# Performance work log

Hardware: AMD Instinct MI355X
Metric: run time of the kernel (lower is better)

## Reference

```python
import jax, jax.numpy as jnp
import numpy as np

# TuckerLinear: in_features = out_features = 4096, num_modes = 3
IN_SHAPE = (16, 16, 16)    # get_shape(4096, 3)
OUT_SHAPE = (16, 16, 16)
IN_FEATURES = 4096
OUT_FEATURES = 4096


def setup_inputs() -> dict:
    key = jax.random.key(0)
    ks = jax.random.split(key, 12)
    B, S = 4, 4096
    x = jax.random.normal(ks[0], (B, S, IN_FEATURES), dtype=jnp.float32)
    core = jax.random.normal(ks[1], (8, 8, 8, 8, 8, 8), dtype=jnp.float32) * 0.05
    fi0 = jax.random.normal(ks[2], (16, 8), dtype=jnp.float32) * 0.3
    fi1 = jax.random.normal(ks[3], (16, 8), dtype=jnp.float32) * 0.3
    fi2 = jax.random.normal(ks[4], (16, 8), dtype=jnp.float32) * 0.3
    fo0 = jax.random.normal(ks[5], (16, 8), dtype=jnp.float32) * 0.3
    fo1 = jax.random.normal(ks[6], (16, 8), dtype=jnp.float32) * 0.3
    fo2 = jax.random.normal(ks[7], (16, 8), dtype=jnp.float32) * 0.3
    bias = jax.random.normal(ks[8], (OUT_FEATURES,), dtype=jnp.float32) * 0.01
    per_dim_scale = jnp.ones((OUT_FEATURES,), dtype=jnp.float32)
    alpha = jnp.ones((1,), dtype=jnp.float32)
    input_perm = jax.random.permutation(ks[9], IN_FEATURES).astype(jnp.int32)
    return dict(x=x, core=core, fi0=fi0, fi1=fi1, fi2=fi2,
                fo0=fo0, fo1=fo1, fo2=fo2,
                per_dim_scale=per_dim_scale, alpha=alpha, bias=bias,
                input_perm=input_perm)


def reference(x, core, fi0, fi1, fi2, fo0, fo1, fo2,
              per_dim_scale, alpha, bias, input_perm):
    batch_dims = x.shape[:-1]
    # 1. input channel permutation (spectral reordering)
    xp = jnp.take(x, input_perm, axis=-1)
    # 2. reshape to expose input modes: (N, 16, 16, 16)
    t = xp.reshape(-1, *IN_SHAPE)
    # 3. contract each input mode with its factor (16 -> 8)
    t = jnp.einsum('nabc,ap->npbc', t, fi0)
    t = jnp.einsum('npbc,bq->npqc', t, fi1)
    t = jnp.einsum('npqc,cr->npqr', t, fi2)
    # 4. contract with core over all input-rank modes: (N,8,8,8) -> (N,8,8,8)
    t = jnp.einsum('npqr,xyzpqr->nxyz', t, core)
    # 5. contract each output mode with its factor (8 -> 16)
    t = jnp.einsum('nxyz,Xx->nXyz', t, fo0)
    t = jnp.einsum('nXyz,Yy->nXYz', t, fo1)
    t = jnp.einsum('nXYz,Zz->nXYZ', t, fo2)
    # 6. flatten output modes, scale, bias
    out = t.reshape(-1, OUT_FEATURES)
    out = out * per_dim_scale * alpha + bias
    return out.reshape(*batch_dims, OUT_FEATURES)
```

## Files before the change

kernel.cpp:

```cpp
#include <hip/hip_runtime.h>
#include <stdint.h>

#define NROWS 16384
#define D 4096

typedef __bf16 bf16x8 __attribute__((ext_vector_type(8)));
typedef float  f32x4  __attribute__((ext_vector_type(4)));

__device__ inline unsigned short f2bf(float f) {
    unsigned u = __float_as_uint(f);
    u += 0x7fffu + ((u >> 16) & 1u);
    return (unsigned short)(u >> 16);
}

__global__ __launch_bounds__(256) void k_corebf(const float* __restrict__ core,
                                                unsigned int* __restrict__ cb) {
    const int o = blockIdx.x;
    const int kp = threadIdx.x;
    float2 v = *(const float2*)&core[o * 512 + 2 * kp];
    cb[((size_t)(kp >> 2) * 512 + o) * 4 + (kp & 3)] =
        (unsigned)f2bf(v.x) | ((unsigned)f2bf(v.y) << 16);
}

__global__ __launch_bounds__(256, 5) void k_t3(const float* __restrict__ x,
                                               const float* __restrict__ fi0,
                                               const float* __restrict__ fi1,
                                               const float* __restrict__ fi2,
                                               const int* __restrict__ perm,
                                               unsigned int* __restrict__ t3out) {
    __shared__ float xr[4096];
    __shared__ float t1[2048];
    __shared__ float t2[1024];
    __shared__ float fac[3][128];

    const int tid = threadIdx.x;
    const int n = blockIdx.x;

    {
        const int h = tid & 127;
        fac[0][h] = fi0[h];
        fac[1][h] = fi1[h];
        fac[2][h] = fi2[h];
    }
    int pj[16];
    #pragma unroll
    for (int j = 0; j < 16; ++j) pj[j] = perm[j * 256 + tid];

    {
        const float4* src = (const float4*)(x + (size_t)n * D);
        #pragma unroll
        for (int i = 0; i < 4; ++i) {
            const int c = i * 256 + tid;
            __builtin_amdgcn_global_load_lds(
                (const __attribute__((address_space(1))) void*)(src + c),
                (__attribute__((address_space(3))) void*)(&xr[c * 4]),
                16, 0, 0);
        }
    }
    asm volatile("s_waitcnt vmcnt(0) lgkmcnt(0)" ::: "memory");
    __builtin_amdgcn_s_barrier();

    {
        float a8[8] = {0,0,0,0,0,0,0,0};
        #pragma unroll
        for (int a = 0; a < 16; ++a) {
            float v = xr[pj[a]];
            #pragma unroll
            for (int p = 0; p < 8; ++p) a8[p] += v * fac[0][a * 8 + p];
        }
        #pragma unroll
        for (int p = 0; p < 8; ++p) t1[p * 256 + tid] = a8[p];
    }
    asm volatile("s_waitcnt lgkmcnt(0)" ::: "memory");
    __builtin_amdgcn_s_barrier();

    {
        const int p = tid >> 5, c = (tid >> 1) & 15, qh = tid & 1;
        float a4[4] = {0,0,0,0};
        #pragma unroll
        for (int b = 0; b < 16; ++b) {
            float v = t1[p * 256 + b * 16 + c];
            #pragma unroll
            for (int qi = 0; qi < 4; ++qi) a4[qi] += v * fac[1][b * 8 + qh * 4 + qi];
        }
        #pragma unroll
        for (int qi = 0; qi < 4; ++qi) t2[p * 128 + (qh * 4 + qi) * 16 + c] = a4[qi];
    }
    asm volatile("s_waitcnt lgkmcnt(0)" ::: "memory");
    __builtin_amdgcn_s_barrier();

    {
        const int p = tid >> 5, q = (tid >> 2) & 7, rh = tid & 3;
        float a2[2] = {0,0};
        #pragma unroll
        for (int c = 0; c < 16; ++c) {
            float v = t2[p * 128 + q * 16 + c];
            #pragma unroll
            for (int ri = 0; ri < 2; ++ri) a2[ri] += v * fac[2][c * 8 + rh * 2 + ri];
        }
        const int kt = tid >> 5, k4 = (tid >> 2) & 7, w = tid & 3;
        t3out[(((size_t)kt * 8 + k4) * NROWS + n) * 4 + w] =
            (unsigned)f2bf(a2[0]) | ((unsigned)f2bf(a2[1]) << 16);
    }
}

__global__ __launch_bounds__(256, 2) void k_core(const __bf16* __restrict__ t3,
                                                 const __bf16* __restrict__ cb,
                                                 unsigned short* __restrict__ t4) {
    __shared__ __bf16 lA[2][8192];
    __shared__ __bf16 lB[2][8192];

    const int tid = threadIdx.x, lane = tid & 63, wv = tid >> 6;

    const int bid = blockIdx.x;
    const int wgid = (bid & 7) * 64 + (bid >> 3);
    const int m0 = (wgid >> 2) * 128;
    const int n0 = (wgid & 3) * 128;
    const int wm = wv >> 1, wn = wv & 1;
    const int l15 = lane & 15, l4 = lane >> 4;

    auto stage = [&](int b, int kt) {
        #pragma unroll
        for (int i = 0; i < 4; ++i) {
            const int c = i * 256 + tid;
            const int k4 = c >> 7, r = c & 127;
            const __bf16* ga = t3 + ((size_t)(kt * 8 + k4) * NROWS + m0 + r) * 8;
            __builtin_amdgcn_global_load_lds(
                (const __attribute__((address_space(1))) void*)ga,
                (__attribute__((address_space(3))) void*)(&lA[b][(size_t)c * 8]),
                16, 0, 0);
            const __bf16* gb = cb + ((size_t)(kt * 8 + k4) * 512 + n0 + r) * 8;
            __builtin_amdgcn_global_load_lds(
                (const __attribute__((address_space(1))) void*)gb,
                (__attribute__((address_space(3))) void*)(&lB[b][(size_t)c * 8]),
                16, 0, 0);
        }
    };

    f32x4 acc[4][4] = {};

    auto compute = [&](int cur) {
        #pragma unroll
        for (int kk = 0; kk < 2; ++kk) {
            const int k4f = kk * 4 + l4;
            bf16x8 af[4], bfr[4];
            #pragma unroll
            for (int mt = 0; mt < 4; ++mt)
                af[mt] = *(const bf16x8*)&lA[cur][(k4f * 128 + wm * 64 + mt * 16 + l15) * 8];
            #pragma unroll
            for (int nt = 0; nt < 4; ++nt)
                bfr[nt] = *(const bf16x8*)&lB[cur][(k4f * 128 + wn * 64 + nt * 16 + l15) * 8];
            #pragma unroll
            for (int mt = 0; mt < 4; ++mt)
                #pragma unroll
                for (int nt = 0; nt < 4; ++nt)
                    acc[mt][nt] = __builtin_amdgcn_mfma_f32_16x16x32_bf16(
                        af[mt], bfr[nt], acc[mt][nt], 0, 0, 0);
        }
    };

    stage(0, 0);
    stage(1, 1);
    #pragma unroll 1
    for (int kt = 0; kt < 8; ++kt) {
        if (kt < 7) asm volatile("s_waitcnt vmcnt(8)" ::: "memory");
        else        asm volatile("s_waitcnt vmcnt(0)" ::: "memory");
        __builtin_amdgcn_s_barrier();
        __builtin_amdgcn_s_setprio(1);
        compute(kt & 1);
        __builtin_amdgcn_s_setprio(0);
        __builtin_amdgcn_s_barrier();
        if (kt < 6) stage(kt & 1, kt + 2);
    }

    #pragma unroll
    for (int nt = 0; nt < 4; ++nt) {
        const int col = n0 + wn * 64 + nt * 16 + l15;
        #pragma unroll
        for (int mt = 0; mt < 4; ++mt) {
            const int row = m0 + wm * 64 + mt * 16 + l4 * 4;
            #pragma unroll
            for (int j = 0; j < 4; ++j)
                t4[(size_t)(row + j) * 512 + col] = f2bf(acc[mt][nt][j]);
        }
    }
}

__global__ __launch_bounds__(256, 3) void k_expand(const unsigned short* __restrict__ t4,
                                                   const float* __restrict__ fo0,
                                                   const float* __restrict__ fo1,
                                                   const float* __restrict__ fo2,
                                                   const float* __restrict__ pds,
                                                   const float* __restrict__ alphap,
                                                   const float* __restrict__ bias,
                                                   float* __restrict__ out) {
    __shared__ unsigned short t4b[4][2][512];
    __shared__ float          t5L[4][1024];
    __shared__ unsigned short t6L[4][2560];
    __shared__ float          fo0L[128];

    const int tid = threadIdx.x, w = tid >> 6, l = tid & 63;
    const int n0 = blockIdx.x * 16 + w * 4;
    const int ly = l >> 3, lz = l & 7;
    const int lq = l & 3, lx = l >> 2;

    if (tid < 128) fo0L[tid] = fo0[tid];
    const float alpha = alphap[0];

    float fo1f[2][8];
    #pragma unroll
    for (int h = 0; h < 2; ++h) {
        f32x4 a = *(const f32x4*)&fo1[(h * 8 + ly) * 8];
        f32x4 b = *(const f32x4*)&fo1[(h * 8 + ly) * 8 + 4];
        #pragma unroll
        for (int j = 0; j < 4; ++j) { fo1f[h][j] = a[j]; fo1f[h][4 + j] = b[j]; }
    }
    float fo2s[4][8];
    #pragma unroll
    for (int j = 0; j < 4; ++j) {
        f32x4 a = *(const f32x4*)&fo2[(lq * 4 + j) * 8];
        f32x4 b = *(const f32x4*)&fo2[(lq * 4 + j) * 8 + 4];
        #pragma unroll
        for (int zz = 0; zz < 4; ++zz) { fo2s[j][zz] = a[zz]; fo2s[j][4 + zz] = b[zz]; }
    }

    auto stage = [&](int b, int n) {
        const unsigned short* src = t4 + (size_t)n * 512 + l * 8;
        __builtin_amdgcn_global_load_lds(
            (const __attribute__((address_space(1))) void*)src,
            (__attribute__((address_space(3))) void*)(&t4b[w][b][l * 8]),
            16, 0, 0);
    };

    stage(0, n0);
    asm volatile("s_waitcnt vmcnt(0) lgkmcnt(0)" ::: "memory");
    __syncthreads();

    #pragma unroll 1
    for (int r = 0; r < 4; ++r) {
        const int b = r & 1;
        if (r) asm volatile("s_waitcnt vmcnt(48)" ::: "memory");

        float rv[8];
        #pragma unroll
        for (int xx = 0; xx < 8; ++xx)
            rv[xx] = __uint_as_float((unsigned)t4b[w][b][xx * 64 + l] << 16);
        if (r + 1 < 4) stage(b ^ 1, n0 + r + 1);
        #pragma unroll
        for (int X = 0; X < 16; ++X) {
            f32x4 f0 = *(const f32x4*)&fo0L[X * 8];
            f32x4 f1 = *(const f32x4*)&fo0L[X * 8 + 4];
            float s = rv[0] * f0[0] + rv[1] * f0[1] + rv[2] * f0[2] + rv[3] * f0[3]
                    + rv[4] * f1[0] + rv[5] * f1[1] + rv[6] * f1[2] + rv[7] * f1[3];
            t5L[w][X * 64 + lz * 8 + ly] = s;
        }
        asm volatile("s_waitcnt lgkmcnt(0)" ::: "memory");

        #pragma unroll
        for (int X = 0; X < 16; ++X) {
            f32x4 u0 = *(const f32x4*)&t5L[w][X * 64 + lz * 8];
            f32x4 u1 = *(const f32x4*)&t5L[w][X * 64 + lz * 8 + 4];
            float a0 = u0[0] * fo1f[0][0] + u0[1] * fo1f[0][1] + u0[2] * fo1f[0][2] + u0[3] * fo1f[0][3]
                     + u1[0] * fo1f[0][4] + u1[1] * fo1f[0][5] + u1[2] * fo1f[0][6] + u1[3] * fo1f[0][7];
            float a1 = u0[0] * fo1f[1][0] + u0[1] * fo1f[1][1] + u0[2] * fo1f[1][2] + u0[3] * fo1f[1][3]
                     + u1[0] * fo1f[1][4] + u1[1] * fo1f[1][5] + u1[2] * fo1f[1][6] + u1[3] * fo1f[1][7];
            t6L[w][(X * 16 + ly) * 10 + lz]     = f2bf(a0);
            t6L[w][(X * 16 + ly + 8) * 10 + lz] = f2bf(a1);
        }
        asm volatile("s_waitcnt lgkmcnt(0)" ::: "memory");

        float* orow = out + (size_t)(n0 + r) * 4096;
        #pragma unroll
        for (int c2 = 0; c2 < 16; ++c2) {
            const int XY = c2 * 16 + lx;
            f32x4 pq = *(const f32x4*)&pds[c2 * 256 + l * 4];
            f32x4 bq = *(const f32x4*)&bias[c2 * 256 + l * 4];
            float tv[8];
            #pragma unroll
            for (int k = 0; k < 4; ++k) {
                unsigned u = *(const unsigned*)&t6L[w][XY * 10 + 2 * k];
                tv[2 * k]     = __uint_as_float(u << 16);
                tv[2 * k + 1] = __uint_as_float(u & 0xffff0000u);
            }
            f32x4 o4;
            #pragma unroll
            for (int j = 0; j < 4; ++j) {
                float t7 = tv[0] * fo2s[j][0] + tv[1] * fo2s[j][1]
                         + tv[2] * fo2s[j][2] + tv[3] * fo2s[j][3]
                         + tv[4] * fo2s[j][4] + tv[5] * fo2s[j][5]
                         + tv[6] * fo2s[j][6] + tv[7] * fo2s[j][7];
                o4[j] = t7 * (pq[j] * alpha) + bq[j];
            }
            *(f32x4*)&orow[c2 * 256 + l * 4] = o4;
        }
        asm volatile("s_waitcnt lgkmcnt(0)" ::: "memory");
    }
}

extern "C" void kernel_launch(void* const* d_in, const int* in_sizes, int n_in,
                              void* d_out, int out_size, void* d_ws, size_t ws_size,
                              hipStream_t stream) {
    const float* x     = (const float*)d_in[0];
    const float* core  = (const float*)d_in[1];
    const float* fi0   = (const float*)d_in[2];
    const float* fi1   = (const float*)d_in[3];
    const float* fi2   = (const float*)d_in[4];
    const float* fo0   = (const float*)d_in[5];
    const float* fo1   = (const float*)d_in[6];
    const float* fo2   = (const float*)d_in[7];
    const float* pds   = (const float*)d_in[8];
    const float* alpha = (const float*)d_in[9];
    const float* bias  = (const float*)d_in[10];
    const int*   perm  = (const int*)d_in[11];
    float* outp = (float*)d_out;

    char* ws = (char*)d_ws;
    unsigned int*   cb   = (unsigned int*)(ws);
    unsigned int*   t3ws = (unsigned int*)(ws + 1048576);
    unsigned short* t4   = (unsigned short*)(ws + 17825792);

    k_corebf<<<512, 256, 0, stream>>>(core, cb);
    k_t3<<<NROWS, 256, 0, stream>>>(x, fi0, fi1, fi2, perm, t3ws);
    k_core<<<512, 256, 0, stream>>>((const __bf16*)t3ws, (const __bf16*)cb, t4);
    k_expand<<<1024, 256, 0, stream>>>(t4, fo0, fo1, fo2, pds, alpha, bias, outp);
}
```

Before: 170.3 us.

## Fuse core GEMM with output-mode expansion, keeping t4 in shared memory

Merges the core-contraction GEMM and the expansion kernel into one kernel. Each block computes a 32-row tile of t4 with MFMA, writes it to LDS, and expands it to the output rows, so the t4 round trip through global memory and one launch go away. The B operand (core) is now read straight from global memory without LDS staging. Scale and bias are preloaded into registers. The risks are fewer blocks (512), high register pressure from the hoisted pds/bias arrays, and no overlap of loads with compute inside the GEMM.

```diff
diff --git a/kernel.cpp b/kernel.cpp
--- a/kernel.cpp
+++ b/kernel.cpp
@@ -104,109 +104,73 @@
     }
 }
 
-__global__ __launch_bounds__(256, 2) void k_core(const __bf16* __restrict__ t3,
-                                                 const __bf16* __restrict__ cb,
-                                                 unsigned short* __restrict__ t4) {
-    __shared__ __bf16 lA[2][8192];
-    __shared__ __bf16 lB[2][8192];
-
-    const int tid = threadIdx.x, lane = tid & 63, wv = tid >> 6;
-
-    const int bid = blockIdx.x;
-    const int wgid = (bid & 7) * 64 + (bid >> 3);
-    const int m0 = (wgid >> 2) * 128;
-    const int n0 = (wgid & 3) * 128;
-    const int wm = wv >> 1, wn = wv & 1;
-    const int l15 = lane & 15, l4 = lane >> 4;
-
-    auto stage = [&](int b, int kt) {
-        #pragma unroll
-        for (int i = 0; i < 4; ++i) {
-            const int c = i * 256 + tid;
-            const int k4 = c >> 7, r = c & 127;
-            const __bf16* ga = t3 + ((size_t)(kt * 8 + k4) * NROWS + m0 + r) * 8;
-            __builtin_amdgcn_global_load_lds(
-                (const __attribute__((address_space(1))) void*)ga,
-                (__attribute__((address_space(3))) void*)(&lA[b][(size_t)c * 8]),
-                16, 0, 0);
-            const __bf16* gb = cb + ((size_t)(kt * 8 + k4) * 512 + n0 + r) * 8;
-            __builtin_amdgcn_global_load_lds(
-                (const __attribute__((address_space(1))) void*)gb,
-                (__attribute__((address_space(3))) void*)(&lB[b][(size_t)c * 8]),
-                16, 0, 0);
-        }
-    };
-
-    f32x4 acc[4][4] = {};
-
-    auto compute = [&](int cur) {
-        #pragma unroll
-        for (int kk = 0; kk < 2; ++kk) {
-            const int k4f = kk * 4 + l4;
-            bf16x8 af[4], bfr[4];
-            #pragma unroll
-            for (int mt = 0; mt < 4; ++mt)
-                af[mt] = *(const bf16x8*)&lA[cur][(k4f * 128 + wm * 64 + mt * 16 + l15) * 8];
-            #pragma unroll
-            for (int nt = 0; nt < 4; ++nt)
-                bfr[nt] = *(const bf16x8*)&lB[cur][(k4f * 128 + wn * 64 + nt * 16 + l15) * 8];
-            #pragma unroll
-            for (int mt = 0; mt < 4; ++mt)
-                #pragma unroll
-                for (int nt = 0; nt < 4; ++nt)
-                    acc[mt][nt] = __builtin_amdgcn_mfma_f32_16x16x32_bf16(
-                        af[mt], bfr[nt], acc[mt][nt], 0, 0, 0);
-        }
-    };
-
-    stage(0, 0);
-    stage(1, 1);
-    #pragma unroll 1
-    for (int kt = 0; kt < 8; ++kt) {
-        if (kt < 7) asm volatile("s_waitcnt vmcnt(8)" ::: "memory");
-        else        asm volatile("s_waitcnt vmcnt(0)" ::: "memory");
-        __builtin_amdgcn_s_barrier();
-        __builtin_amdgcn_s_setprio(1);
-        compute(kt & 1);
-        __builtin_amdgcn_s_setprio(0);
-        __builtin_amdgcn_s_barrier();
-        if (kt < 6) stage(kt & 1, kt + 2);
-    }
-
-    #pragma unroll
-    for (int nt = 0; nt < 4; ++nt) {
-        const int col = n0 + wn * 64 + nt * 16 + l15;
-        #pragma unroll
-        for (int mt = 0; mt < 4; ++mt) {
-            const int row = m0 + wm * 64 + mt * 16 + l4 * 4;
-            #pragma unroll
-            for (int j = 0; j < 4; ++j)
-                t4[(size_t)(row + j) * 512 + col] = f2bf(acc[mt][nt][j]);
-        }
-    }
-}
-
-__global__ __launch_bounds__(256, 3) void k_expand(const unsigned short* __restrict__ t4,
-                                                   const float* __restrict__ fo0,
-                                                   const float* __restrict__ fo1,
-                                                   const float* __restrict__ fo2,
-                                                   const float* __restrict__ pds,
-                                                   const float* __restrict__ alphap,
-                                                   const float* __restrict__ bias,
-                                                   float* __restrict__ out) {
-    __shared__ unsigned short t4b[4][2][512];
+__global__ __launch_bounds__(256, 2) void k_ce(const __bf16* __restrict__ t3,
+                                               const __bf16* __restrict__ cb,
+                                               const float* __restrict__ fo0,
+                                               const float* __restrict__ fo1,
+                                               const float* __restrict__ fo2,
+                                               const float* __restrict__ pds,
+                                               const float* __restrict__ alphap,
+                                               const float* __restrict__ bias,
+                                               float* __restrict__ out) {
+    __shared__ __attribute__((aligned(16))) __bf16 smemA[16384];
     __shared__ float          t5L[4][1024];
     __shared__ unsigned short t6L[4][2560];
     __shared__ float          fo0L[128];
 
     const int tid = threadIdx.x, w = tid >> 6, l = tid & 63;
-    const int n0 = blockIdx.x * 16 + w * 4;
+    const int n0 = blockIdx.x * 32;
+    const int l15 = l & 15, l4 = l >> 4;
     const int ly = l >> 3, lz = l & 7;
     const int lq = l & 3, lx = l >> 2;
 
     if (tid < 128) fo0L[tid] = fo0[tid];
+
+    #pragma unroll
+    for (int i = 0; i < 8; ++i) {
+        const int c = i * 256 + tid;
+        const int kq = c >> 5, r = c & 31;
+        const __bf16* ga = t3 + ((size_t)kq * NROWS + n0 + r) * 8;
+        __builtin_amdgcn_global_load_lds(
+            (const __attribute__((address_space(1))) void*)ga,
+            (__attribute__((address_space(3))) void*)(smemA + (size_t)c * 8),
+            16, 0, 0);
+    }
+    asm volatile("s_waitcnt vmcnt(0) lgkmcnt(0)" ::: "memory");
+    __builtin_amdgcn_s_barrier();
+
+    f32x4 acc[2][8] = {};
+    #pragma unroll 2
+    for (int kk = 0; kk < 16; ++kk) {
+        const int kq = kk * 4 + l4;
+        bf16x8 af0 = *(const bf16x8*)&smemA[((kq) * 32 + l15) * 8];
+        bf16x8 af1 = *(const bf16x8*)&smemA[((kq) * 32 + 16 + l15) * 8];
+        #pragma unroll
+        for (int nt = 0; nt < 8; ++nt) {
+            bf16x8 bv = *(const bf16x8*)(cb + ((size_t)kq * 512 + w * 128 + nt * 16 + l15) * 8);
+            acc[0][nt] = __builtin_amdgcn_mfma_f32_16x16x32_bf16(af0, bv, acc[0][nt], 0, 0, 0);
+            acc[1][nt] = __builtin_amdgcn_mfma_f32_16x16x32_bf16(af1, bv, acc[1][nt], 0, 0, 0);
+        }
+    }
+
+    asm volatile("s_waitcnt lgkmcnt(0)" ::: "memory");
+    __builtin_amdgcn_s_barrier();
+
+    {
+        unsigned short* t4w = (unsigned short*)smemA;
+        #pragma unroll
+        for (int mt = 0; mt < 2; ++mt)
+            #pragma unroll
+            for (int nt = 0; nt < 8; ++nt)
+                #pragma unroll
+                for (int j = 0; j < 4; ++j)
+                    t4w[(mt * 16 + l4 * 4 + j) * 512 + w * 128 + nt * 16 + l15] =
+                        f2bf(acc[mt][nt][j]);
+    }
+    asm volatile("s_waitcnt lgkmcnt(0)" ::: "memory");
+    __builtin_amdgcn_s_barrier();
+
     const float alpha = alphap[0];
-
     float fo1f[2][8];
     #pragma unroll
     for (int h = 0; h < 2; ++h) {
@@ -223,29 +187,25 @@
         #pragma unroll
         for (int zz = 0; zz < 4; ++zz) { fo2s[j][zz] = a[zz]; fo2s[j][4 + zz] = b[zz]; }
     }
-
-    auto stage = [&](int b, int n) {
-        const unsigned short* src = t4 + (size_t)n * 512 + l * 8;
-        __builtin_amdgcn_global_load_lds(
-            (const __attribute__((address_space(1))) void*)src,
-            (__attribute__((address_space(3))) void*)(&t4b[w][b][l * 8]),
-            16, 0, 0);
-    };
-
-    stage(0, n0);
-    asm volatile("s_waitcnt vmcnt(0) lgkmcnt(0)" ::: "memory");
-    __syncthreads();
+    f32x4 pqr[16], bqr[16];
+    #pragma unroll
+    for (int c2 = 0; c2 < 16; ++c2) {
+        f32x4 p = *(const f32x4*)&pds[c2 * 256 + l * 4];
+        pqr[c2][0] = p[0] * alpha; pqr[c2][1] = p[1] * alpha;
+        pqr[c2][2] = p[2] * alpha; pqr[c2][3] = p[3] * alpha;
+        bqr[c2] = *(const f32x4*)&bias[c2 * 256 + l * 4];
+    }
+
+    const unsigned short* t4b = (const unsigned short*)smemA;
 
     #pragma unroll 1
-    for (int r = 0; r < 4; ++r) {
-        const int b = r & 1;
-        if (r) asm volatile("s_waitcnt vmcnt(48)" ::: "memory");
+    for (int rr = 0; rr < 8; ++rr) {
+        const int row = w * 8 + rr;
 
         float rv[8];
         #pragma unroll
         for (int xx = 0; xx < 8; ++xx)
-            rv[xx] = __uint_as_float((unsigned)t4b[w][b][xx * 64 + l] << 16);
-        if (r + 1 < 4) stage(b ^ 1, n0 + r + 1);
+            rv[xx] = __uint_as_float((unsigned)t4b[row * 512 + xx * 64 + l] << 16);
         #pragma unroll
         for (int X = 0; X < 16; ++X) {
             f32x4 f0 = *(const f32x4*)&fo0L[X * 8];
@@ -269,12 +229,10 @@
         }
         asm volatile("s_waitcnt lgkmcnt(0)" ::: "memory");
 
-        float* orow = out + (size_t)(n0 + r) * 4096;
+        float* orow = out + (size_t)(n0 + row) * 4096;
         #pragma unroll
         for (int c2 = 0; c2 < 16; ++c2) {
             const int XY = c2 * 16 + lx;
-            f32x4 pq = *(const f32x4*)&pds[c2 * 256 + l * 4];
-            f32x4 bq = *(const f32x4*)&bias[c2 * 256 + l * 4];
             float tv[8];
             #pragma unroll
             for (int k = 0; k < 4; ++k) {
@@ -289,7 +247,7 @@
                          + tv[2] * fo2s[j][2] + tv[3] * fo2s[j][3]
                          + tv[4] * fo2s[j][4] + tv[5] * fo2s[j][5]
                          + tv[6] * fo2s[j][6] + tv[7] * fo2s[j][7];
-                o4[j] = t7 * (pq[j] * alpha) + bq[j];
+                o4[j] = t7 * pqr[c2][j] + bqr[c2][j];
             }
             *(f32x4*)&orow[c2 * 256 + l * 4] = o4;
         }
@@ -315,12 +273,11 @@
     float* outp = (float*)d_out;
 
     char* ws = (char*)d_ws;
-    unsigned int*   cb   = (unsigned int*)(ws);
-    unsigned int*   t3ws = (unsigned int*)(ws + 1048576);
-    unsigned short* t4   = (unsigned short*)(ws + 17825792);
+    unsigned int* cb   = (unsigned int*)(ws);
+    unsigned int* t3ws = (unsigned int*)(ws + 1048576);
 
     k_corebf<<<512, 256, 0, stream>>>(core, cb);
     k_t3<<<NROWS, 256, 0, stream>>>(x, fi0, fi1, fi2, perm, t3ws);
-    k_core<<<512, 256, 0, stream>>>((const __bf16*)t3ws, (const __bf16*)cb, t4);
-    k_expand<<<1024, 256, 0, stream>>>(t4, fo0, fo1, fo2, pds, alpha, bias, outp);
-}
+    k_ce<<<512, 256, 0, stream>>>((const __bf16*)t3ws, (const __bf16*)cb,
+                                  fo0, fo1, fo2, pds, alpha, bias, outp);
+}
```

After: 171.0 us. About the same (+0.4%).
